# Kernel optimization log

Measured on AMD Instinct MI355X. Metric: run time of the kernel, lower is better.

## Reference

```python
import jax, jax.numpy as jnp
import numpy as np
import math

IN_CH = 1024
OUT_CH = 1024
QK_DIM = 512
NHEADS = 8
NDIM = QK_DIM // NHEADS  # 64 per-head qk dim
VDIM = OUT_CH // NHEADS  # 128 per-head value dim
SCALE = 1.0 / math.sqrt(NDIM)


def setup_inputs() -> dict:
    key = jax.random.key(0)
    ks = jax.random.split(key, 7)
    B, N = 4, 2048
    x = jax.random.normal(ks[0], (B, N, IN_CH), dtype=jnp.float32)
    # Linear weights stored as [in, out] so y = x @ W + b
    s_in = 1.0 / math.sqrt(IN_CH)
    Wq = jax.random.uniform(ks[1], (IN_CH, QK_DIM), jnp.float32, -s_in, s_in)
    bq = jax.random.uniform(ks[2], (QK_DIM,), jnp.float32, -s_in, s_in)
    Wk = jax.random.uniform(ks[3], (IN_CH, QK_DIM), jnp.float32, -s_in, s_in)
    bk = jax.random.uniform(ks[4], (QK_DIM,), jnp.float32, -s_in, s_in)
    Wv = jax.random.uniform(ks[5], (IN_CH, OUT_CH), jnp.float32, -s_in, s_in)
    bv = jax.random.uniform(ks[6], (OUT_CH,), jnp.float32, -s_in, s_in)
    return {"x": x, "Wq": Wq, "bq": bq, "Wk": Wk, "bk": bk, "Wv": Wv, "bv": bv}


def reference(x, Wq, bq, Wk, bk, Wv, bv):
    B, N, C = x.shape
    Q = (x @ Wq + bq).reshape(B, N, NHEADS, NDIM)
    K = (x @ Wk + bk).reshape(B, N, NHEADS, NDIM)
    V = (x @ Wv + bv).reshape(B, N, NHEADS, VDIM)
    # scores: [B, H, N, N]
    scores = jnp.einsum("bnhd,bmhd->bhnm", Q, K) * SCALE
    attn = jax.nn.softmax(scores, axis=-1)
    # message: [B, N, H, VDIM] -> [B, N, OUT_CH]
    msg = jnp.einsum("bhnm,bmhv->bnhv", attn, V)
    return msg.reshape(B, N, OUT_CH)
```

## Files before the change

kernel.cpp:

```cpp
#include <hip/hip_runtime.h>
#include <hip/hip_bf16.h>
#include <math.h>


using bf16 = __hip_bfloat16;
typedef __attribute__((ext_vector_type(8))) short short8;
typedef __attribute__((ext_vector_type(4))) float f32x4;
typedef __attribute__((ext_vector_type(16))) float f32x16;

#define C2 0.18033688011112042f

__device__ __forceinline__ void async_ld16(const void* g, void* l) {
  __builtin_amdgcn_global_load_lds(
      (const __attribute__((address_space(1))) unsigned int*)g,
      (__attribute__((address_space(3))) unsigned int*)l, 16, 0, 0);
}

__global__ __launch_bounds__(256) void convert_x(const float* __restrict__ x,
                                                 bf16* __restrict__ xb)
{
  const int i = (blockIdx.x * 256 + threadIdx.x) * 8;
  const float4 a = *(const float4*)(x + i);
  const float4 b = *(const float4*)(x + i + 4);
  union { bf16 h[8]; short8 s; } u;
  u.h[0] = __float2bfloat16(a.x); u.h[1] = __float2bfloat16(a.y);
  u.h[2] = __float2bfloat16(a.z); u.h[3] = __float2bfloat16(a.w);
  u.h[4] = __float2bfloat16(b.x); u.h[5] = __float2bfloat16(b.y);
  u.h[6] = __float2bfloat16(b.z); u.h[7] = __float2bfloat16(b.w);
  *(short8*)(xb + i) = u.s;
}

__global__ __launch_bounds__(256) void transpose_weights(
    const float* __restrict__ Wq, const float* __restrict__ Wk,
    const float* __restrict__ Wv, bf16* __restrict__ Wt)
{
  __shared__ __align__(16) bf16 t[32][33];
  const int i0 = blockIdx.x * 32;
  const int o0 = blockIdx.y * 32;
  const int tx = threadIdx.x & 31, ty = threadIdx.x >> 5;
#pragma unroll
  for (int s = 0; s < 32; s += 8) {
    const int i = i0 + ty + s;
    const int o = o0 + tx;
    const float w = (o < 512)  ? Wq[(size_t)i * 512 + o]
                  : (o < 1024) ? Wk[(size_t)i * 512 + (o - 512)]
                               : Wv[(size_t)i * 1024 + (o - 1024)];
    t[ty + s][tx] = __float2bfloat16(w);
  }
  __syncthreads();
#pragma unroll
  for (int s = 0; s < 32; s += 8)
    Wt[(size_t)(o0 + ty + s) * 1024 + i0 + tx] = t[tx][ty + s];
}

__global__ __launch_bounds__(256, 2) void qkv_gemm(
    const bf16* __restrict__ xb, const bf16* __restrict__ Wt,
    const float* __restrict__ bq, const float* __restrict__ bk,
    const float* __restrict__ bv, bf16* __restrict__ QKV)
{
  __shared__ __align__(16) bf16 As[128 * 64];
  __shared__ __align__(16) bf16 Bs[128 * 64];
  const int tid = threadIdx.x;
  const int w = tid >> 6, lane = tid & 63, quad = lane >> 4, l16 = lane & 15;
  const int m0 = blockIdx.y * 128, n0 = blockIdx.x * 128;
  const int wm = (w >> 1) * 64, wn = (w & 1) * 64;
  f32x4 acc[4][4];
  const f32x4 z4 = {0.f, 0.f, 0.f, 0.f};
#pragma unroll
  for (int mi = 0; mi < 4; ++mi)
#pragma unroll
    for (int ni = 0; ni < 4; ++ni) acc[mi][ni] = z4;

  for (int k0 = 0; k0 < 1024; k0 += 64) {
    __syncthreads();
#pragma unroll
    for (int it = 0; it < 4; ++it) {
      const int L = it * 256 + tid;
      const int row = L >> 3;
      const int c16 = (L & 7) ^ (row & 7);
      async_ld16(xb + (size_t)(m0 + row) * 1024 + k0 + c16 * 8, &As[L * 8]);
      async_ld16(Wt + (size_t)(n0 + row) * 1024 + k0 + c16 * 8, &Bs[L * 8]);
    }
    __syncthreads();
#pragma unroll
    for (int kk = 0; kk < 2; ++kk) {
      short8 af[4], bfr[4];
#pragma unroll
      for (int mi = 0; mi < 4; ++mi) {
        const int row = wm + mi * 16 + l16;
        const int p = ((kk << 2) | quad) ^ (row & 7);
        af[mi] = *(const short8*)&As[row * 64 + p * 8];
      }
#pragma unroll
      for (int ni = 0; ni < 4; ++ni) {
        const int row = wn + ni * 16 + l16;
        const int p = ((kk << 2) | quad) ^ (row & 7);
        bfr[ni] = *(const short8*)&Bs[row * 64 + p * 8];
      }
#pragma unroll
      for (int mi = 0; mi < 4; ++mi)
#pragma unroll
        for (int ni = 0; ni < 4; ++ni)
          acc[mi][ni] = __builtin_amdgcn_mfma_f32_16x16x32_bf16(af[mi], bfr[ni], acc[mi][ni], 0, 0, 0);
    }
  }
#pragma unroll
  for (int ni = 0; ni < 4; ++ni) {
    const int colg = n0 + wn + ni * 16 + l16;
    const float bias = colg < 512 ? bq[colg]
                     : (colg < 1024 ? bk[colg - 512] : bv[colg - 1024]);
    const float scl = (colg >= 512 && colg < 1024) ? C2 : 1.0f;
#pragma unroll
    for (int mi = 0; mi < 4; ++mi)
#pragma unroll
      for (int reg = 0; reg < 4; ++reg) {
        const int rowg = m0 + wm + mi * 16 + quad * 4 + reg;
        QKV[(size_t)rowg * 2048 + colg] = __float2bfloat16((acc[mi][ni][reg] + bias) * scl);
      }
  }
}

__global__ __launch_bounds__(256) void transpose_v(
    const bf16* __restrict__ QKV, bf16* __restrict__ Vt)
{
  __shared__ __align__(16) bf16 t[32][33];
  const int r0 = blockIdx.x * 32;
  const int c0 = blockIdx.y * 32;
  const int tx = threadIdx.x & 31, ty = threadIdx.x >> 5;
#pragma unroll
  for (int s = 0; s < 32; s += 8)
    t[ty + s][tx] = QKV[(size_t)(r0 + ty + s) * 2048 + 1024 + c0 + tx];
  __syncthreads();
#pragma unroll
  for (int s = 0; s < 32; s += 8)
    Vt[(size_t)(c0 + ty + s) * 8192 + r0 + tx] = t[tx][ty + s];
}

__global__ __launch_bounds__(256, 2) void flash_attn(
    const bf16* __restrict__ QKV, const bf16* __restrict__ Vt, float* __restrict__ out)
{
  __shared__ __align__(16) bf16 smem[128 * 64 + 128 * 128];
  bf16* Ks = smem;
  bf16* Vs = smem + 128 * 64;
  const int tid = threadIdx.x;
  const int w = tid >> 6, lane = tid & 63, l31 = lane & 31, hi = lane >> 5;
  const int q0 = blockIdx.x * 128;
  const int h  = blockIdx.y;
  const size_t tb = (size_t)blockIdx.z * 2048;

  short8 qf[4];
  const int qrow = w * 32 + l31;
  const bf16* qptr = QKV + (tb + q0 + qrow) * 2048 + h * 64 + hi * 8;
#pragma unroll
  for (int dd = 0; dd < 4; ++dd)
    qf[dd] = *(const short8*)(qptr + dd * 16);

  f32x16 O[4];
#pragma unroll
  for (int t = 0; t < 4; ++t)
#pragma unroll
    for (int e = 0; e < 16; ++e) O[t][e] = 0.f;
  float l_run = 0.f;

  for (int k0 = 0; k0 < 2048; k0 += 128) {
    __syncthreads();
#pragma unroll
    for (int it = 0; it < 4; ++it) {
      const int L = it * 256 + tid;
      const int row = L >> 3;
      const int c16 = (L & 7) ^ (row & 7);
      async_ld16(QKV + (tb + k0 + row) * 2048 + 512 + h * 64 + c16 * 8, &Ks[L * 8]);
    }
#pragma unroll
    for (int it = 0; it < 8; ++it) {
      const int L = it * 256 + tid;
      const int row = L >> 4;
      const int c16 = (L & 15) ^ (row & 15);
      async_ld16(Vt + (size_t)(h * 128 + row) * 8192 + tb + k0 + c16 * 8, &Vs[L * 8]);
    }
    __syncthreads();

    float rsum = 0.f;
#pragma unroll
    for (int kt = 0; kt < 4; ++kt) {
      f32x16 S;
#pragma unroll
      for (int e = 0; e < 16; ++e) S[e] = 0.f;
      const int krow = kt * 32 + l31;
#pragma unroll
      for (int d = 0; d < 4; ++d) {
        const int p = (2 * d + hi) ^ (krow & 7);
        const short8 kf = *(const short8*)&Ks[krow * 64 + p * 8];
        S = __builtin_amdgcn_mfma_f32_32x32x16_bf16(kf, qf[d], S, 0, 0, 0);
      }
      unsigned int pk[8];
#pragma unroll
      for (int dw = 0; dw < 8; ++dw) {
        const float p0 = exp2f(S[2 * dw]);
        const float p1 = exp2f(S[2 * dw + 1]);
        rsum += p0 + p1;
        union { bf16 hh[2]; unsigned int u; } cc;
        cc.hh[0] = __float2bfloat16(p0); cc.hh[1] = __float2bfloat16(p1);
        pk[dw] = cc.u;
      }
#pragma unroll
      for (int half = 0; half < 2; ++half) {
        const int c16 = 2 * kt + half;
        const int b4 = half * 4;
        const unsigned int lo0 = pk[b4],     lo1 = pk[b4 + 1];
        const unsigned int up0 = pk[b4 + 2], up1 = pk[b4 + 3];
        const unsigned int s0 = hi ? lo0 : up0, s1 = hi ? lo1 : up1;
        const unsigned int r0 = (unsigned int)__shfl_xor((int)s0, 32, 64);
        const unsigned int r1 = (unsigned int)__shfl_xor((int)s1, 32, 64);
        union { unsigned int d[4]; short8 v; } pf;
        pf.d[0] = hi ? r0 : lo0;  pf.d[1] = hi ? r1 : lo1;
        pf.d[2] = hi ? up0 : r0;  pf.d[3] = hi ? up1 : r1;
#pragma unroll
        for (int vt = 0; vt < 4; ++vt) {
          const int vrow = vt * 32 + l31;
          const int p = (2 * c16 + hi) ^ (vrow & 15);
          const short8 vf = *(const short8*)&Vs[vrow * 128 + p * 8];
          O[vt] = __builtin_amdgcn_mfma_f32_32x32x16_bf16(vf, pf.v, O[vt], 0, 0, 0);
        }
      }
    }
    rsum += __shfl_xor(rsum, 32, 64);
    l_run += rsum;
  }

  const float inv_l = 1.0f / l_run;
  float* tbuf = (float*)smem;
  const int qg = tid >> 1;
  const int part = tid & 1;
  for (int vt = 0; vt < 4; ++vt) {
    __syncthreads();
#pragma unroll
    for (int e = 0; e < 16; ++e) {
      const int vl = (e & 3) + 8 * (e >> 2) + 4 * hi;
      tbuf[vl * 132 + w * 32 + l31] = O[vt][e] * inv_l;
    }
    __syncthreads();
    float* dst = out + (tb + q0 + qg) * 1024 + h * 128 + vt * 32 + part * 16;
#pragma unroll
    for (int i = 0; i < 4; ++i) {
      float4 v4;
      v4.x = tbuf[(part * 16 + 4 * i + 0) * 132 + qg];
      v4.y = tbuf[(part * 16 + 4 * i + 1) * 132 + qg];
      v4.z = tbuf[(part * 16 + 4 * i + 2) * 132 + qg];
      v4.w = tbuf[(part * 16 + 4 * i + 3) * 132 + qg];
      *(float4*)(dst + 4 * i) = v4;
    }
  }
}

extern "C" void kernel_launch(void* const* d_in, const int* in_sizes, int n_in,
                              void* d_out, int out_size, void* d_ws, size_t ws_size,
                              hipStream_t stream) {
  const float* x  = (const float*)d_in[0];
  const float* Wq = (const float*)d_in[1];
  const float* bq = (const float*)d_in[2];
  const float* Wk = (const float*)d_in[3];
  const float* bk = (const float*)d_in[4];
  const float* Wv = (const float*)d_in[5];
  const float* bv = (const float*)d_in[6];
  float* out = (float*)d_out;

  char* ws = (char*)d_ws;
  bf16* QKV = (bf16*)ws;
  bf16* Vt  = (bf16*)(ws + 33554432);
  bf16* Wt  = (bf16*)(ws + 33554432 + 16777216);
  bf16* xb  = (bf16*)(ws + 33554432 + 16777216 + 4194304);

  convert_x<<<dim3(4096), 256, 0, stream>>>(x, xb);
  transpose_weights<<<dim3(32, 64), 256, 0, stream>>>(Wq, Wk, Wv, Wt);
  qkv_gemm<<<dim3(16, 64), 256, 0, stream>>>(xb, Wt, bq, bk, bv, QKV);
  transpose_v<<<dim3(256, 32), 256, 0, stream>>>(QKV, Vt);
  flash_attn<<<dim3(16, 8, 4), 256, 0, stream>>>(QKV, Vt, out);
}
```

Measured before the change: 222.5 us.

## Double-buffer K/V tiles with 64-key stages and use permlane32 swap

```diff
diff --git a/kernel.cpp b/kernel.cpp
--- a/kernel.cpp
+++ b/kernel.cpp
@@ -7,6 +7,7 @@
 typedef __attribute__((ext_vector_type(8))) short short8;
 typedef __attribute__((ext_vector_type(4))) float f32x4;
 typedef __attribute__((ext_vector_type(16))) float f32x16;
+typedef __attribute__((ext_vector_type(2))) unsigned int uintx2;
 
 #define C2 0.18033688011112042f
 
@@ -139,9 +140,7 @@
 __global__ __launch_bounds__(256, 2) void flash_attn(
     const bf16* __restrict__ QKV, const bf16* __restrict__ Vt, float* __restrict__ out)
 {
-  __shared__ __align__(16) bf16 smem[128 * 64 + 128 * 128];
-  bf16* Ks = smem;
-  bf16* Vs = smem + 128 * 64;
+  __shared__ __align__(16) bf16 smem[2 * 4096 + 2 * 8192];
   const int tid = threadIdx.x;
   const int w = tid >> 6, lane = tid & 63, l31 = lane & 31, hi = lane >> 5;
   const int q0 = blockIdx.x * 128;
@@ -155,6 +154,21 @@
   for (int dd = 0; dd < 4; ++dd)
     qf[dd] = *(const short8*)(qptr + dd * 16);
 
+  const bf16* kg[2]; int kld[2];
+#pragma unroll
+  for (int it = 0; it < 2; ++it) {
+    const int L = it * 256 + tid, row = L >> 3, c = (L & 7) ^ (row & 7);
+    kg[it] = QKV + (tb + row) * 2048 + 512 + h * 64 + c * 8;
+    kld[it] = L * 8;
+  }
+  const bf16* vg[4]; int vld[4];
+#pragma unroll
+  for (int it = 0; it < 4; ++it) {
+    const int L = it * 256 + tid, row = L >> 3, c = (L & 7) ^ (row & 7);
+    vg[it] = Vt + (size_t)(h * 128 + row) * 8192 + tb + c * 8;
+    vld[it] = L * 8;
+  }
+
   f32x16 O[4];
 #pragma unroll
   for (int t = 0; t < 4; ++t)
@@ -162,27 +176,25 @@
     for (int e = 0; e < 16; ++e) O[t][e] = 0.f;
   float l_run = 0.f;
 
-  for (int k0 = 0; k0 < 2048; k0 += 128) {
-    __syncthreads();
-#pragma unroll
-    for (int it = 0; it < 4; ++it) {
-      const int L = it * 256 + tid;
-      const int row = L >> 3;
-      const int c16 = (L & 7) ^ (row & 7);
-      async_ld16(QKV + (tb + k0 + row) * 2048 + 512 + h * 64 + c16 * 8, &Ks[L * 8]);
-    }
-#pragma unroll
-    for (int it = 0; it < 8; ++it) {
-      const int L = it * 256 + tid;
-      const int row = L >> 4;
-      const int c16 = (L & 15) ^ (row & 15);
-      async_ld16(Vt + (size_t)(h * 128 + row) * 8192 + tb + k0 + c16 * 8, &Vs[L * 8]);
-    }
-    __syncthreads();
-
+  auto stage = [&](int buf) {
+#pragma unroll
+    for (int i = 0; i < 2; ++i) {
+      async_ld16(kg[i], &smem[buf * 4096 + kld[i]]);
+      kg[i] += 64 * 2048;
+    }
+#pragma unroll
+    for (int i = 0; i < 4; ++i) {
+      async_ld16(vg[i], &smem[8192 + buf * 8192 + vld[i]]);
+      vg[i] += 64;
+    }
+  };
+
+  auto compute = [&](int buf) {
+    const bf16* Kb = smem + buf * 4096;
+    const bf16* Vb = smem + 8192 + buf * 8192;
     float rsum = 0.f;
 #pragma unroll
-    for (int kt = 0; kt < 4; ++kt) {
+    for (int kt = 0; kt < 2; ++kt) {
       f32x16 S;
 #pragma unroll
       for (int e = 0; e < 16; ++e) S[e] = 0.f;
@@ -190,7 +202,7 @@
 #pragma unroll
       for (int d = 0; d < 4; ++d) {
         const int p = (2 * d + hi) ^ (krow & 7);
-        const short8 kf = *(const short8*)&Ks[krow * 64 + p * 8];
+        const short8 kf = *(const short8*)&Kb[krow * 64 + p * 8];
         S = __builtin_amdgcn_mfma_f32_32x32x16_bf16(kf, qf[d], S, 0, 0, 0);
       }
       unsigned int pk[8];
@@ -205,28 +217,38 @@
       }
 #pragma unroll
       for (int half = 0; half < 2; ++half) {
-        const int c16 = 2 * kt + half;
+        const int kc = 2 * kt + half;
         const int b4 = half * 4;
-        const unsigned int lo0 = pk[b4],     lo1 = pk[b4 + 1];
-        const unsigned int up0 = pk[b4 + 2], up1 = pk[b4 + 3];
-        const unsigned int s0 = hi ? lo0 : up0, s1 = hi ? lo1 : up1;
-        const unsigned int r0 = (unsigned int)__shfl_xor((int)s0, 32, 64);
-        const unsigned int r1 = (unsigned int)__shfl_xor((int)s1, 32, 64);
+        const uintx2 s0 = __builtin_amdgcn_permlane32_swap(pk[b4],     pk[b4 + 2], false, false);
+        const uintx2 s1 = __builtin_amdgcn_permlane32_swap(pk[b4 + 1], pk[b4 + 3], false, false);
         union { unsigned int d[4]; short8 v; } pf;
-        pf.d[0] = hi ? r0 : lo0;  pf.d[1] = hi ? r1 : lo1;
-        pf.d[2] = hi ? up0 : r0;  pf.d[3] = hi ? up1 : r1;
+        pf.d[0] = s0.x; pf.d[1] = s1.x; pf.d[2] = s0.y; pf.d[3] = s1.y;
 #pragma unroll
         for (int vt = 0; vt < 4; ++vt) {
           const int vrow = vt * 32 + l31;
-          const int p = (2 * c16 + hi) ^ (vrow & 15);
-          const short8 vf = *(const short8*)&Vs[vrow * 128 + p * 8];
+          const int p = (2 * kc + hi) ^ (vrow & 7);
+          const short8 vf = *(const short8*)&Vb[vrow * 64 + p * 8];
           O[vt] = __builtin_amdgcn_mfma_f32_32x32x16_bf16(vf, pf.v, O[vt], 0, 0, 0);
         }
       }
     }
-    rsum += __shfl_xor(rsum, 32, 64);
     l_run += rsum;
-  }
+  };
+
+  stage(0);
+  __syncthreads();
+  int cur = 0;
+  for (int t = 0; t < 31; ++t) {
+    stage(cur ^ 1);
+    __builtin_amdgcn_s_setprio(1);
+    compute(cur);
+    __builtin_amdgcn_s_setprio(0);
+    __syncthreads();
+    cur ^= 1;
+  }
+  compute(cur);
+
+  l_run += __shfl_xor(l_run, 32, 64);
 
   const float inv_l = 1.0f / l_run;
   float* tbuf = (float*)smem;
```

Measured after the change: 217.5 us. 1.02x faster.

## Triple-buffer K/V tiles with async loads and permlane32 swaps in flash attention

Applied to the files above, without the earlier changes.

```diff
diff --git a/kernel.cpp b/kernel.cpp
--- a/kernel.cpp
+++ b/kernel.cpp
@@ -7,6 +7,7 @@
 typedef __attribute__((ext_vector_type(8))) short short8;
 typedef __attribute__((ext_vector_type(4))) float f32x4;
 typedef __attribute__((ext_vector_type(16))) float f32x16;
+typedef __attribute__((ext_vector_type(2))) unsigned int uintx2;
 
 #define C2 0.18033688011112042f
 
@@ -139,9 +140,8 @@
 __global__ __launch_bounds__(256, 2) void flash_attn(
     const bf16* __restrict__ QKV, const bf16* __restrict__ Vt, float* __restrict__ out)
 {
-  __shared__ __align__(16) bf16 smem[128 * 64 + 128 * 128];
-  bf16* Ks = smem;
-  bf16* Vs = smem + 128 * 64;
+  __shared__ __align__(16) bf16 smem[3 * 12288];
+  char* smemc = (char*)smem;
   const int tid = threadIdx.x;
   const int w = tid >> 6, lane = tid & 63, l31 = lane & 31, hi = lane >> 5;
   const int q0 = blockIdx.x * 128;
@@ -155,78 +155,113 @@
   for (int dd = 0; dd < 4; ++dd)
     qf[dd] = *(const short8*)(qptr + dd * 16);
 
+  int adr[4];
+#pragma unroll
+  for (int i = 0; i < 4; ++i)
+    adr[i] = l31 * 128 + (((2 * i + hi) ^ (l31 & 7)) * 16);
+
+  const bf16* kg[2]; int kldo[2];
+#pragma unroll
+  for (int i = 0; i < 2; ++i) {
+    const int L = i * 256 + tid, row = L >> 3, c = (L & 7) ^ (row & 7);
+    kg[i] = QKV + (tb + row) * 2048 + 512 + h * 64 + c * 8;
+    kldo[i] = L * 16;
+  }
+  const bf16* vg[4]; int vldo[4];
+#pragma unroll
+  for (int i = 0; i < 4; ++i) {
+    const int L = i * 256 + tid, row = L >> 3, c = (L & 7) ^ (row & 7);
+    vg[i] = Vt + (size_t)(h * 128 + row) * 8192 + tb + c * 8;
+    vldo[i] = L * 16;
+  }
+
   f32x16 O[4];
 #pragma unroll
   for (int t = 0; t < 4; ++t)
 #pragma unroll
     for (int e = 0; e < 16; ++e) O[t][e] = 0.f;
-  float l_run = 0.f;
-
-  for (int k0 = 0; k0 < 2048; k0 += 128) {
-    __syncthreads();
-#pragma unroll
-    for (int it = 0; it < 4; ++it) {
-      const int L = it * 256 + tid;
-      const int row = L >> 3;
-      const int c16 = (L & 7) ^ (row & 7);
-      async_ld16(QKV + (tb + k0 + row) * 2048 + 512 + h * 64 + c16 * 8, &Ks[L * 8]);
-    }
-#pragma unroll
-    for (int it = 0; it < 8; ++it) {
-      const int L = it * 256 + tid;
-      const int row = L >> 4;
-      const int c16 = (L & 15) ^ (row & 15);
-      async_ld16(Vt + (size_t)(h * 128 + row) * 8192 + tb + k0 + c16 * 8, &Vs[L * 8]);
-    }
-    __syncthreads();
-
-    float rsum = 0.f;
-#pragma unroll
-    for (int kt = 0; kt < 4; ++kt) {
-      f32x16 S;
-#pragma unroll
-      for (int e = 0; e < 16; ++e) S[e] = 0.f;
-      const int krow = kt * 32 + l31;
-#pragma unroll
-      for (int d = 0; d < 4; ++d) {
-        const int p = (2 * d + hi) ^ (krow & 7);
-        const short8 kf = *(const short8*)&Ks[krow * 64 + p * 8];
-        S = __builtin_amdgcn_mfma_f32_32x32x16_bf16(kf, qf[d], S, 0, 0, 0);
-      }
-      unsigned int pk[8];
-#pragma unroll
-      for (int dw = 0; dw < 8; ++dw) {
-        const float p0 = exp2f(S[2 * dw]);
-        const float p1 = exp2f(S[2 * dw + 1]);
-        rsum += p0 + p1;
-        union { bf16 hh[2]; unsigned int u; } cc;
-        cc.hh[0] = __float2bfloat16(p0); cc.hh[1] = __float2bfloat16(p1);
-        pk[dw] = cc.u;
-      }
-#pragma unroll
-      for (int half = 0; half < 2; ++half) {
-        const int c16 = 2 * kt + half;
-        const int b4 = half * 4;
-        const unsigned int lo0 = pk[b4],     lo1 = pk[b4 + 1];
-        const unsigned int up0 = pk[b4 + 2], up1 = pk[b4 + 3];
-        const unsigned int s0 = hi ? lo0 : up0, s1 = hi ? lo1 : up1;
-        const unsigned int r0 = (unsigned int)__shfl_xor((int)s0, 32, 64);
-        const unsigned int r1 = (unsigned int)__shfl_xor((int)s1, 32, 64);
-        union { unsigned int d[4]; short8 v; } pf;
-        pf.d[0] = hi ? r0 : lo0;  pf.d[1] = hi ? r1 : lo1;
-        pf.d[2] = hi ? up0 : r0;  pf.d[3] = hi ? up1 : r1;
-#pragma unroll
-        for (int vt = 0; vt < 4; ++vt) {
-          const int vrow = vt * 32 + l31;
-          const int p = (2 * c16 + hi) ^ (vrow & 15);
-          const short8 vf = *(const short8*)&Vs[vrow * 128 + p * 8];
-          O[vt] = __builtin_amdgcn_mfma_f32_32x32x16_bf16(vf, pf.v, O[vt], 0, 0, 0);
-        }
-      }
-    }
-    rsum += __shfl_xor(rsum, 32, 64);
-    l_run += rsum;
-  }
+  f32x16 Z;
+#pragma unroll
+  for (int e = 0; e < 16; ++e) Z[e] = 0.f;
+  float2 rs; rs.x = 0.f; rs.y = 0.f;
+
+#define STAGE(B) do {                                                        \
+  _Pragma("unroll") for (int i = 0; i < 2; ++i) {                            \
+    async_ld16(kg[i], smemc + (B) * 24576 + kldo[i]); kg[i] += 131072; }     \
+  _Pragma("unroll") for (int i = 0; i < 4; ++i) {                            \
+    async_ld16(vg[i], smemc + (B) * 24576 + 8192 + vldo[i]); vg[i] += 64; }  \
+} while (0)
+
+#define SOFTPV(B, KT, SV) do {                                               \
+  unsigned int pk[8];                                                        \
+  _Pragma("unroll") for (int dw = 0; dw < 8; ++dw) {                         \
+    const float e0 = exp2f(SV[2 * dw]);                                      \
+    const float e1 = exp2f(SV[2 * dw + 1]);                                  \
+    rs.x += e0; rs.y += e1;                                                  \
+    union { bf16 hh[2]; unsigned int u; } cc;                                \
+    cc.hh[0] = __float2bfloat16(e0); cc.hh[1] = __float2bfloat16(e1);        \
+    pk[dw] = cc.u; }                                                         \
+  _Pragma("unroll") for (int half = 0; half < 2; ++half) {                   \
+    const int kc = 2 * (KT) + half; const int b4 = half * 4;                 \
+    const uintx2 s0 = __builtin_amdgcn_permlane32_swap(pk[b4], pk[b4 + 2], false, false);     \
+    const uintx2 s1 = __builtin_amdgcn_permlane32_swap(pk[b4 + 1], pk[b4 + 3], false, false); \
+    union { unsigned int d[4]; short8 v; } pf;                               \
+    pf.d[0] = s0.x; pf.d[1] = s1.x; pf.d[2] = s0.y; pf.d[3] = s1.y;          \
+    _Pragma("unroll") for (int vt = 0; vt < 4; ++vt) {                       \
+      const short8 vf = *(const short8*)(smemc + (B) * 24576 + 8192 + vt * 4096 + adr[kc]); \
+      O[vt] = __builtin_amdgcn_mfma_f32_32x32x16_bf16(vf, pf.v, O[vt], 0, 0, 0); } }        \
+} while (0)
+
+#define COMPUTE(B) do {                                                      \
+  __builtin_amdgcn_s_setprio(1);                                            \
+  short8 kf; f32x16 S0, S1;                                                  \
+  kf = *(const short8*)(smemc + (B) * 24576 + adr[0]);                       \
+  S0 = __builtin_amdgcn_mfma_f32_32x32x16_bf16(kf, qf[0], Z, 0, 0, 0);       \
+  kf = *(const short8*)(smemc + (B) * 24576 + adr[1]);                       \
+  S0 = __builtin_amdgcn_mfma_f32_32x32x16_bf16(kf, qf[1], S0, 0, 0, 0);      \
+  kf = *(const short8*)(smemc + (B) * 24576 + adr[2]);                       \
+  S0 = __builtin_amdgcn_mfma_f32_32x32x16_bf16(kf, qf[2], S0, 0, 0, 0);      \
+  kf = *(const short8*)(smemc + (B) * 24576 + adr[3]);                       \
+  S0 = __builtin_amdgcn_mfma_f32_32x32x16_bf16(kf, qf[3], S0, 0, 0, 0);      \
+  kf = *(const short8*)(smemc + (B) * 24576 + 4096 + adr[0]);                \
+  S1 = __builtin_amdgcn_mfma_f32_32x32x16_bf16(kf, qf[0], Z, 0, 0, 0);       \
+  kf = *(const short8*)(smemc + (B) * 24576 + 4096 + adr[1]);                \
+  S1 = __builtin_amdgcn_mfma_f32_32x32x16_bf16(kf, qf[1], S1, 0, 0, 0);      \
+  kf = *(const short8*)(smemc + (B) * 24576 + 4096 + adr[2]);                \
+  S1 = __builtin_amdgcn_mfma_f32_32x32x16_bf16(kf, qf[2], S1, 0, 0, 0);      \
+  kf = *(const short8*)(smemc + (B) * 24576 + 4096 + adr[3]);                \
+  S1 = __builtin_amdgcn_mfma_f32_32x32x16_bf16(kf, qf[3], S1, 0, 0, 0);      \
+  SOFTPV(B, 0, S0);                                                          \
+  SOFTPV(B, 1, S1);                                                          \
+  __builtin_amdgcn_s_setprio(0);                                            \
+} while (0)
+
+#define PIPE_SYNC6 do {                                                      \
+  asm volatile("s_waitcnt vmcnt(6)" ::: "memory");                           \
+  __builtin_amdgcn_s_barrier();                                              \
+  __builtin_amdgcn_sched_barrier(0);                                         \
+} while (0)
+
+  STAGE(0); STAGE(1);
+  PIPE_SYNC6;
+  for (int u = 0; u < 10; ++u) {
+    STAGE(2); COMPUTE(0); PIPE_SYNC6;
+    STAGE(0); COMPUTE(1); PIPE_SYNC6;
+    STAGE(1); COMPUTE(2); PIPE_SYNC6;
+  }
+  COMPUTE(0);
+  asm volatile("s_waitcnt vmcnt(0)" ::: "memory");
+  __builtin_amdgcn_s_barrier();
+  __builtin_amdgcn_sched_barrier(0);
+  COMPUTE(1);
+
+#undef STAGE
+#undef SOFTPV
+#undef COMPUTE
+#undef PIPE_SYNC6
+
+  float l_run = rs.x + rs.y;
+  l_run += __shfl_xor(l_run, 32, 64);
 
   const float inv_l = 1.0f / l_run;
   float* tbuf = (float*)smem;
```

Measured after the change: 226.9 us. No clear change (+2.0%).
